# Kernel optimization log

Hardware: AMD Instinct MI355X
Metric: run time of the kernel (lower is better)

## Reference

```python
import math
import jax, jax.numpy as jnp
import numpy as np

NUM_HEADS = 16

def _alibi_slopes(n):
    def pow2(n):
        start = 2 ** (-2 ** (-(math.log2(n) - 3)))
        return [start * start ** i for i in range(n)]
    if math.log2(n).is_integer():
        return pow2(n)
    c = 2 ** math.floor(math.log2(n))
    return pow2(c) + _alibi_slopes(2 * c)[0::2][: n - c]

def _alibi_bias(num_heads, L):
    pos = np.arange(L)
    rel = (pos[None, :] - pos[:, None]).astype(np.float32)  # [L, L]
    slopes = np.asarray(_alibi_slopes(num_heads), dtype=np.float32)[:, None, None]
    bias = slopes * rel[None, :, :]  # [H, L, L]
    causal = pos[None, :] <= pos[:, None]
    bias = np.where(causal[None, :, :], bias, -np.inf).astype(np.float32)
    return jnp.asarray(bias)[None]  # [1, H, L, L]

def setup_inputs() -> dict:
    key = jax.random.key(0)
    ks = jax.random.split(key, 4)
    B, L, D = 2, 2048, 1024
    x = jax.random.normal(ks[0], (B, L, D), dtype=jnp.float32)
    W_in = jax.random.normal(ks[1], (D, 3 * D), dtype=jnp.float32) * 0.02
    b_in = jnp.zeros((3 * D,), dtype=jnp.float32)
    W_out = jax.random.normal(ks[2], (D, D), dtype=jnp.float32) * 0.02
    b_out = jnp.zeros((D,), dtype=jnp.float32)
    return {"x": x, "W_in": W_in, "b_in": b_in, "W_out": W_out, "b_out": b_out}

def reference(x, W_in, b_in, W_out, b_out):
    B, L, D = x.shape
    H = NUM_HEADS
    Dh = D // H
    qkv = x @ W_in + b_in  # [B, L, 3D]
    q, k, v = jnp.split(qkv, 3, axis=-1)
    # [B, H, L, Dh]
    q = q.reshape(B, L, H, Dh).transpose(0, 2, 1, 3)
    k = k.reshape(B, L, H, Dh).transpose(0, 2, 1, 3)
    v = v.reshape(B, L, H, Dh).transpose(0, 2, 1, 3)
    attn = jnp.einsum("bhqd,bhkd->bhqk", q, k) * (1.0 / math.sqrt(Dh))
    attn = attn + _alibi_bias(H, L)  # ALiBi + causal mask (-inf above diag)
    p = jax.nn.softmax(attn, axis=-1)
    out = jnp.einsum("bhqk,bhkd->bhqd", p, v)
    out = out.transpose(0, 2, 1, 3).reshape(B, L, D)
    out = out @ W_out + b_out
    return out, k, v
```

## Files before the change

kernel.cpp:

```cpp
#include <hip/hip_runtime.h>
#include <math.h>

typedef __bf16 bf16x8 __attribute__((ext_vector_type(8)));
typedef float  f32x4  __attribute__((ext_vector_type(4)));
typedef unsigned short u16x4 __attribute__((ext_vector_type(4)));

#define BATCH  2
#define SEQ    2048
#define DMODEL 1024
#define NHEAD  16
#define DHEAD  64
#define MROWS  4096
#define N_QKV  3072
#define KDIM   1024
#define OUTSECT (MROWS*DMODEL)

#define LOG2E 1.44269504088896f
#define QSCALE (0.125f * LOG2E)

__device__ inline __bf16 f2bf(float f) {
    unsigned u = __builtin_bit_cast(unsigned, f);
    unsigned r = (u + 0x7fffu + ((u >> 16) & 1u)) >> 16;
    return __builtin_bit_cast(__bf16, (unsigned short)r);
}

__device__ inline void gload16(const void* g, void* l) {
    __builtin_amdgcn_global_load_lds(
        (const __attribute__((address_space(1))) void*)g,
        (__attribute__((address_space(3))) void*)l, 16, 0, 0);
}

__device__ inline float dpp_max16(float x) {
    int v, t;
    v = __builtin_bit_cast(int, x);
    t = __builtin_amdgcn_update_dpp(v, v, 0xB1, 0xF, 0xF, false);
    x = fmaxf(x, __builtin_bit_cast(float, t));
    v = __builtin_bit_cast(int, x);
    t = __builtin_amdgcn_update_dpp(v, v, 0x4E, 0xF, 0xF, false);
    x = fmaxf(x, __builtin_bit_cast(float, t));
    v = __builtin_bit_cast(int, x);
    t = __builtin_amdgcn_update_dpp(v, v, 0x128, 0xF, 0xF, false);
    x = fmaxf(x, __builtin_bit_cast(float, t));
    v = __builtin_bit_cast(int, x);
    t = __builtin_amdgcn_update_dpp(v, v, 0x140, 0xF, 0xF, false);
    x = fmaxf(x, __builtin_bit_cast(float, t));
    return x;
}
__device__ inline float dpp_sum16(float x) {
    int v, t;
    v = __builtin_bit_cast(int, x);
    t = __builtin_amdgcn_update_dpp(v, v, 0xB1, 0xF, 0xF, false);
    x += __builtin_bit_cast(float, t);
    v = __builtin_bit_cast(int, x);
    t = __builtin_amdgcn_update_dpp(v, v, 0x4E, 0xF, 0xF, false);
    x += __builtin_bit_cast(float, t);
    v = __builtin_bit_cast(int, x);
    t = __builtin_amdgcn_update_dpp(v, v, 0x128, 0xF, 0xF, false);
    x += __builtin_bit_cast(float, t);
    v = __builtin_bit_cast(int, x);
    t = __builtin_amdgcn_update_dpp(v, v, 0x140, 0xF, 0xF, false);
    x += __builtin_bit_cast(float, t);
    return x;
}

__global__ __launch_bounds__(256) void cvt_all_k(
    const float* __restrict__ x, __bf16* __restrict__ xb,
    const float* __restrict__ W_in, __bf16* __restrict__ wti,
    const float* __restrict__ W_out, __bf16* __restrict__ wto)
{
    __shared__ float t[64][65];
    const int b = blockIdx.x;
    const int tid = threadIdx.x;
    if (b < 2048) {
        size_t i = (size_t)b * 256 + tid;
        const float4* p = (const float4*)x + i * 2;
        float4 a = p[0], c = p[1];
        __bf16 o[8] = {f2bf(a.x), f2bf(a.y), f2bf(a.z), f2bf(a.w),
                       f2bf(c.x), f2bf(c.y), f2bf(c.z), f2bf(c.w)};
        *(bf16x8*)(xb + i * 8) = *(bf16x8*)o;
        return;
    }
    const float* W;  __bf16* Wt;  int Nw, bx, by;
    if (b < 2816) { int c = b - 2048; W = W_in;  Wt = wti; Nw = N_QKV;  bx = c % 48; by = c / 48; }
    else          { int c = b - 2816; W = W_out; Wt = wto; Nw = DMODEL; bx = c % 16; by = c / 16; }
    const int k0 = by * 64, n0 = bx * 64;
    #pragma unroll
    for (int u = 0; u < 4; ++u) {
        int idx = u * 256 + tid;
        int r = idx >> 4, c4 = (idx & 15) << 2;
        float4 v = *(const float4*)&W[(size_t)(k0 + r) * Nw + n0 + c4];
        t[r][c4] = v.x; t[r][c4 + 1] = v.y; t[r][c4 + 2] = v.z; t[r][c4 + 3] = v.w;
    }
    __syncthreads();
    #pragma unroll
    for (int u = 0; u < 2; ++u) {
        int idx = u * 256 + tid;
        int n = idx >> 3, k8 = (idx & 7) << 3;
        __bf16 o[8];
        #pragma unroll
        for (int i = 0; i < 8; ++i) o[i] = f2bf(t[k8 + i][n]);
        *(bf16x8*)&Wt[(size_t)(n0 + n) * KDIM + k0 + k8] = *(bf16x8*)o;
    }
}

template<int MODE, int FI, int FJ>
__global__ __launch_bounds__(256) void gemm_bf(
    const __bf16* __restrict__ A, const __bf16* __restrict__ Bt,
    const float* __restrict__ bias,
    float* __restrict__ fo, float* __restrict__ kf, float* __restrict__ vf,
    __bf16* __restrict__ qb, __bf16* __restrict__ kb, __bf16* __restrict__ vb,
    int nbx)
{
    constexpr int BMt = FI * 32, BNt = FJ * 32;
    __shared__ __align__(16) __bf16 As[BMt * 64];
    __shared__ __align__(16) __bf16 Bs[BNt * 64];

    const int tid = threadIdx.x, wid = tid >> 6, lane = tid & 63;
    const int l16 = lane & 15, lq = lane >> 4;
    const int wm = wid >> 1, wn = wid & 1;

    const int nwg = gridDim.x;
    const int bid = blockIdx.x;
    const int swz = (bid & 7) * (nwg >> 3) + (bid >> 3);
    const int m0 = (swz / nbx) * BMt;
    const int n0 = (swz % nbx) * BNt;

    const int lr8 = lane >> 3;
    const int colE = ((lane & 7) ^ lr8) << 3;

    f32x4 acc[FI][FJ];
    #pragma unroll
    for (int i = 0; i < FI; ++i)
        #pragma unroll
        for (int j = 0; j < FJ; ++j)
            acc[i][j] = f32x4{0.f, 0.f, 0.f, 0.f};

    for (int k0 = 0; k0 < KDIM; k0 += 64) {
        __syncthreads();
        #pragma unroll
        for (int c = wid; c < FI * 4 + FJ * 4; c += 4) {
            const bool isA = (c < FI * 4);
            const int ch = isA ? c : c - FI * 4;
            const int row = ch * 8 + lr8;
            const __bf16* src = isA ? (A  + (size_t)(m0 + row) * KDIM + k0 + colE)
                                    : (Bt + (size_t)(n0 + row) * KDIM + k0 + colE);
            gload16(src, (isA ? As : Bs) + ch * 512);
        }
        __syncthreads();
        #pragma unroll
        for (int kk = 0; kk < 2; ++kk) {
            bf16x8 af[FI], bfg[FJ];
            #pragma unroll
            for (int i = 0; i < FI; ++i) {
                int r = wm * (FI * 16) + i * 16 + l16;
                af[i] = *(const bf16x8*)&As[r * 64 + ((kk * 32 + lq * 8) ^ ((r & 7) << 3))];
            }
            #pragma unroll
            for (int j = 0; j < FJ; ++j) {
                int r = wn * (FJ * 16) + j * 16 + l16;
                bfg[j] = *(const bf16x8*)&Bs[r * 64 + ((kk * 32 + lq * 8) ^ ((r & 7) << 3))];
            }
            #pragma unroll
            for (int i = 0; i < FI; ++i)
                #pragma unroll
                for (int j = 0; j < FJ; ++j)
                    acc[i][j] = __builtin_amdgcn_mfma_f32_16x16x32_bf16(af[i], bfg[j], acc[i][j], 0, 0, 0);
        }
    }

    #pragma unroll
    for (int i = 0; i < FI; ++i) {
        #pragma unroll
        for (int j = 0; j < FJ; ++j) {
            const int col  = n0 + wn * (FJ * 16) + j * 16 + l16;
            const int rowb = m0 + wm * (FI * 16) + i * 16 + lq * 4;
            float v[4];
            #pragma unroll
            for (int r = 0; r < 4; ++r) v[r] = acc[i][j][r] + bias[col];
            if (MODE == 1) {
                #pragma unroll
                for (int r = 0; r < 4; ++r)
                    fo[(size_t)(rowb + r) * DMODEL + col] = v[r];
            } else {
                const int which = col >> 10, rem = col & 1023;
                const int h = rem >> 6, dh = rem & 63;
                const int bb = rowb >> 11, ll = rowb & 2047;
                const size_t lidx = ((size_t)(bb * NHEAD + h) * SEQ + ll) * DHEAD + dh;
                if (which == 0) {
                    #pragma unroll
                    for (int r = 0; r < 4; ++r)
                        qb[lidx + (size_t)r * DHEAD] = f2bf(v[r] * QSCALE);
                } else if (which == 1) {
                    #pragma unroll
                    for (int r = 0; r < 4; ++r) {
                        kf[lidx + (size_t)r * DHEAD] = v[r];
                        kb[lidx + (size_t)r * DHEAD] = f2bf(v[r]);
                    }
                } else {
                    u16x4 pk;
                    #pragma unroll
                    for (int r = 0; r < 4; ++r) {
                        vf[lidx + (size_t)r * DHEAD] = v[r];
                        pk[r] = __builtin_bit_cast(unsigned short, f2bf(v[r]));
                    }
                    *(u16x4*)&vb[((size_t)(bb * NHEAD + h) * DHEAD + dh) * SEQ + ll] = pk;
                }
            }
        }
    }
}

__global__ __launch_bounds__(256) void attn_k(
    const __bf16* __restrict__ Qb, const __bf16* __restrict__ Kb,
    const __bf16* __restrict__ Vb, __bf16* __restrict__ Ob)
{
    __shared__ __align__(16) __bf16 Qs[64 * 64];
    __shared__ __align__(16) __bf16 Ks[2][64 * 64];
    __shared__ __align__(16) __bf16 Vs[2][64 * 64];
    __shared__ __align__(16) __bf16 Ps[4 * 16 * 64];

    const int tid = threadIdx.x, wid = tid >> 6, lane = tid & 63;
    const int l16 = lane & 15, lq = lane >> 4;

    const int bid = blockIdx.x;
    const int t   = bid >> 3;
    const int qt  = 31 - (t >> 2);
    const int bh  = (bid & 7) * 4 + (t & 3);
    const int h = bh & 15, bb = bh >> 4;
    const int q0 = qt * 64;
    const size_t kvbase = (size_t)bh * SEQ * DHEAD;
    const float slope2 = exp2f(-0.5f * (float)(h + 1)) * LOG2E;
    const int qr0 = wid * 16;
    const int lr8 = lane >> 3;
    const int colE = ((lane & 7) ^ lr8) << 3;

    #pragma unroll
    for (int u = 0; u < 2; ++u) {
        int ch = u * 4 + wid;
        int row = ch * 8 + lr8;
        gload16(Qb + kvbase + (size_t)(q0 + row) * DHEAD + colE, Qs + ch * 512);
    }
    #pragma unroll
    for (int u = 0; u < 2; ++u) {
        int ch = u * 4 + wid;
        int row = ch * 8 + lr8;
        gload16(Kb + kvbase + (size_t)row * DHEAD + colE, Ks[0] + ch * 512);
        gload16(Vb + kvbase + (size_t)row * SEQ  + colE, Vs[0] + ch * 512);
    }
    __syncthreads();

    float ct[4][4];
    #pragma unroll
    for (int r = 0; r < 4; ++r) {
        const int qi = q0 + qr0 + lq * 4 + r;
        #pragma unroll
        for (int nf = 0; nf < 4; ++nf)
            ct[r][nf] = slope2 * (float)(nf * 16 + l16 - qi);
    }
    const float dtj = slope2 * 64.f;

    float mrow[4], lrow[4];
    f32x4 accO[4];
    #pragma unroll
    for (int r = 0; r < 4; ++r) { mrow[r] = -1e30f; lrow[r] = 0.f; }
    #pragma unroll
    for (int j = 0; j < 4; ++j) accO[j] = f32x4{0.f, 0.f, 0.f, 0.f};

    int cur = 0;
    for (int jt = 0; jt <= qt; ++jt) {
        if (jt < qt) {
            const int jn = (jt + 1) * 64;
            #pragma unroll
            for (int u = 0; u < 2; ++u) {
                int ch = u * 4 + wid;
                int row = ch * 8 + lr8;
                gload16(Kb + kvbase + (size_t)(jn + row) * DHEAD + colE, Ks[cur ^ 1] + ch * 512);
                gload16(Vb + kvbase + (size_t)row * SEQ + jn + colE,     Vs[cur ^ 1] + ch * 512);
            }
        }

        const float tb = dtj * (float)jt;
        f32x4 s[4];
        #pragma unroll
        for (int nf = 0; nf < 4; ++nf) {
            #pragma unroll
            for (int r = 0; r < 4; ++r) s[nf][r] = ct[r][nf] + tb;
        }
        if (jt == qt) {
            #pragma unroll
            for (int nf = 0; nf < 4; ++nf)
                #pragma unroll
                for (int r = 0; r < 4; ++r)
                    if (nf * 16 + l16 > qr0 + lq * 4 + r) s[nf][r] = -3e38f;
        }

        const int qrow = qr0 + l16;
        bf16x8 aq0 = *(const bf16x8*)&Qs[qrow * 64 + ((lq * 8) ^ ((qrow & 7) << 3))];
        bf16x8 aq1 = *(const bf16x8*)&Qs[qrow * 64 + ((32 + lq * 8) ^ ((qrow & 7) << 3))];
        __builtin_amdgcn_s_setprio(1);
        #pragma unroll
        for (int nf = 0; nf < 4; ++nf) {
            int kr = nf * 16 + l16;
            bf16x8 bk0 = *(const bf16x8*)&Ks[cur][kr * 64 + ((lq * 8) ^ ((kr & 7) << 3))];
            bf16x8 bk1 = *(const bf16x8*)&Ks[cur][kr * 64 + ((32 + lq * 8) ^ ((kr & 7) << 3))];
            s[nf] = __builtin_amdgcn_mfma_f32_16x16x32_bf16(aq0, bk0, s[nf], 0, 0, 0);
            s[nf] = __builtin_amdgcn_mfma_f32_16x16x32_bf16(aq1, bk1, s[nf], 0, 0, 0);
        }
        __builtin_amdgcn_s_setprio(0);

        float rm[4];
        #pragma unroll
        for (int r = 0; r < 4; ++r)
            rm[r] = dpp_max16(fmaxf(fmaxf(s[0][r], s[1][r]), fmaxf(s[2][r], s[3][r])));
        bool need = (rm[0] > mrow[0] + 8.f) || (rm[1] > mrow[1] + 8.f) ||
                    (rm[2] > mrow[2] + 8.f) || (rm[3] > mrow[3] + 8.f);
        if (__any(need)) {
            #pragma unroll
            for (int r = 0; r < 4; ++r) {
                float mnew = fmaxf(mrow[r], rm[r]);
                float scale = __builtin_amdgcn_exp2f(mrow[r] - mnew);
                lrow[r] *= scale;
                mrow[r] = mnew;
                #pragma unroll
                for (int nf = 0; nf < 4; ++nf) accO[nf][r] *= scale;
            }
        }
        #pragma unroll
        for (int r = 0; r < 4; ++r) {
            float p0 = __builtin_amdgcn_exp2f(s[0][r] - mrow[r]);
            float p1 = __builtin_amdgcn_exp2f(s[1][r] - mrow[r]);
            float p2 = __builtin_amdgcn_exp2f(s[2][r] - mrow[r]);
            float p3 = __builtin_amdgcn_exp2f(s[3][r] - mrow[r]);
            const int prow = lq * 4 + r;
            const int pb = wid * 1024 + prow * 64;
            const int px = (prow & 7) << 3;
            Ps[pb + ((l16     ) ^ px)] = (__bf16)p0;
            Ps[pb + ((l16 + 16) ^ px)] = (__bf16)p1;
            Ps[pb + ((l16 + 32) ^ px)] = (__bf16)p2;
            Ps[pb + ((l16 + 48) ^ px)] = (__bf16)p3;
            lrow[r] += dpp_sum16((p0 + p1) + (p2 + p3));
        }

        bf16x8 ap0 = *(const bf16x8*)&Ps[wid * 1024 + l16 * 64 + ((lq * 8) ^ ((l16 & 7) << 3))];
        bf16x8 ap1 = *(const bf16x8*)&Ps[wid * 1024 + l16 * 64 + ((32 + lq * 8) ^ ((l16 & 7) << 3))];
        __builtin_amdgcn_s_setprio(1);
        #pragma unroll
        for (int nf = 0; nf < 4; ++nf) {
            int vr = nf * 16 + l16;
            bf16x8 bv0 = *(const bf16x8*)&Vs[cur][vr * 64 + ((lq * 8) ^ ((vr & 7) << 3))];
            bf16x8 bv1 = *(const bf16x8*)&Vs[cur][vr * 64 + ((32 + lq * 8) ^ ((vr & 7) << 3))];
            accO[nf] = __builtin_amdgcn_mfma_f32_16x16x32_bf16(ap0, bv0, accO[nf], 0, 0, 0);
            accO[nf] = __builtin_amdgcn_mfma_f32_16x16x32_bf16(ap1, bv1, accO[nf], 0, 0, 0);
        }
        __builtin_amdgcn_s_setprio(0);

        __syncthreads();
        cur ^= 1;
    }

    #pragma unroll
    for (int r = 0; r < 4; ++r) {
        const float inv = __builtin_amdgcn_rcpf(lrow[r]);
        const int qi = q0 + qr0 + lq * 4 + r;
        #pragma unroll
        for (int nf = 0; nf < 4; ++nf) {
            int dh = nf * 16 + l16;
            Ob[(size_t)(bb * SEQ + qi) * DMODEL + h * DHEAD + dh] = (__bf16)(accO[nf][r] * inv);
        }
    }
}

extern "C" void kernel_launch(void* const* d_in, const int* in_sizes, int n_in,
                              void* d_out, int out_size, void* d_ws, size_t ws_size,
                              hipStream_t stream) {
    const float* x     = (const float*)d_in[0];
    const float* W_in  = (const float*)d_in[1];
    const float* b_in  = (const float*)d_in[2];
    const float* W_out = (const float*)d_in[3];
    const float* b_out = (const float*)d_in[4];

    float* out = (float*)d_out;
    float* kf  = out + (size_t)OUTSECT;
    float* vf  = out + 2 * (size_t)OUTSECT;

    __bf16* qb = (__bf16*)d_out;
    __bf16* xb = (__bf16*)d_out + (size_t)OUTSECT;

    __bf16* ob  = (__bf16*)d_ws;
    __bf16* kb  = ob + (size_t)OUTSECT;
    __bf16* vb  = kb + (size_t)OUTSECT;
    __bf16* wti = vb + (size_t)OUTSECT;
    __bf16* wto = wti + (size_t)N_QKV * KDIM;

    cvt_all_k<<<3072, 256, 0, stream>>>(x, xb, W_in, wti, W_out, wto);

    gemm_bf<0, 4, 4><<<768, 256, 0, stream>>>(xb, wti, b_in,
        nullptr, kf, vf, qb, kb, vb, N_QKV / 128);

    attn_k<<<1024, 256, 0, stream>>>(qb, kb, vb, ob);

    gemm_bf<1, 4, 4><<<256, 256, 0, stream>>>(ob, wto, b_out,
        out, nullptr, nullptr, nullptr, nullptr, nullptr, DMODEL / 128);
}
```

Baseline: 199.9 us.

## Use 128-row query tiles with 8 waves sharing each K/V tile

The attention kernel now processes 128 query rows per block with 512 threads (8 waves), so each loaded K/V tile is reused by twice as many query rows. This halves global K/V traffic per query. The block schedule pairs a long and a short query tile (half flag) to balance causal work. Q fragments are hoisted out of the loop, and waves whose rows lie entirely above the current key tile skip compute but still join the barrier, which leaves some idle waves on the diagonal tiles.

```diff
diff --git a/kernel.cpp b/kernel.cpp
--- a/kernel.cpp
+++ b/kernel.cpp
@@ -210,49 +210,54 @@
     }
 }
 
-__global__ __launch_bounds__(256) void attn_k(
+__global__ __launch_bounds__(512) void attn_k(
     const __bf16* __restrict__ Qb, const __bf16* __restrict__ Kb,
     const __bf16* __restrict__ Vb, __bf16* __restrict__ Ob)
 {
-    __shared__ __align__(16) __bf16 Qs[64 * 64];
+    __shared__ __align__(16) __bf16 Qs[128 * 64];
     __shared__ __align__(16) __bf16 Ks[2][64 * 64];
     __shared__ __align__(16) __bf16 Vs[2][64 * 64];
-    __shared__ __align__(16) __bf16 Ps[4 * 16 * 64];
+    __shared__ __align__(16) __bf16 Ps[8 * 16 * 64];
 
     const int tid = threadIdx.x, wid = tid >> 6, lane = tid & 63;
     const int l16 = lane & 15, lq = lane >> 4;
 
     const int bid = blockIdx.x;
-    const int t   = bid >> 3;
-    const int qt  = 31 - (t >> 2);
-    const int bh  = (bid & 7) * 4 + (t & 3);
+    const int j   = bid >> 3;
+    const int p   = j >> 1, half = j & 1;
+    const int bh  = (bid & 7) * 4 + (p & 3);
+    const int q2i = p >> 2;
+    const int qt2 = half ? q2i : (15 - q2i);
     const int h = bh & 15, bb = bh >> 4;
-    const int q0 = qt * 64;
+    const int q0b  = qt2 * 128;
+    const int jtop = 2 * qt2 + 1;
     const size_t kvbase = (size_t)bh * SEQ * DHEAD;
     const float slope2 = exp2f(-0.5f * (float)(h + 1)) * LOG2E;
-    const int qr0 = wid * 16;
+    const int qa = q0b + wid * 16;
     const int lr8 = lane >> 3;
     const int colE = ((lane & 7) ^ lr8) << 3;
 
     #pragma unroll
     for (int u = 0; u < 2; ++u) {
-        int ch = u * 4 + wid;
+        int ch = wid * 2 + u;
         int row = ch * 8 + lr8;
-        gload16(Qb + kvbase + (size_t)(q0 + row) * DHEAD + colE, Qs + ch * 512);
-    }
-    #pragma unroll
-    for (int u = 0; u < 2; ++u) {
-        int ch = u * 4 + wid;
-        int row = ch * 8 + lr8;
-        gload16(Kb + kvbase + (size_t)row * DHEAD + colE, Ks[0] + ch * 512);
-        gload16(Vb + kvbase + (size_t)row * SEQ  + colE, Vs[0] + ch * 512);
+        gload16(Qb + kvbase + (size_t)(q0b + row) * DHEAD + colE, Qs + ch * 512);
+    }
+    {
+        int row = wid * 8 + lr8;
+        gload16(Kb + kvbase + (size_t)row * DHEAD + colE, Ks[0] + wid * 512);
+        gload16(Vb + kvbase + (size_t)row * SEQ  + colE, Vs[0] + wid * 512);
     }
     __syncthreads();
 
+    const int qrow = wid * 16 + l16;
+    const bf16x8 aq0 = *(const bf16x8*)&Qs[qrow * 64 + ((lq * 8) ^ ((qrow & 7) << 3))];
+    const bf16x8 aq1 = *(const bf16x8*)&Qs[qrow * 64 + ((32 + lq * 8) ^ ((qrow & 7) << 3))];
+
     float ct[4][4];
     #pragma unroll
     for (int r = 0; r < 4; ++r) {
-        const int qi = q0 + qr0 + lq * 4 + r;
+        const int qi = qa + lq * 4 + r;
         #pragma unroll
         for (int nf = 0; nf < 4; ++nf)
             ct[r][nf] = slope2 * (float)(nf * 16 + l16 - qi);
@@ -264,95 +269,92 @@
     #pragma unroll
     for (int r = 0; r < 4; ++r) { mrow[r] = -1e30f; lrow[r] = 0.f; }
     #pragma unroll
-    for (int j = 0; j < 4; ++j) accO[j] = f32x4{0.f, 0.f, 0.f, 0.f};
+    for (int jj = 0; jj < 4; ++jj) accO[jj] = f32x4{0.f, 0.f, 0.f, 0.f};
 
     int cur = 0;
-    for (int jt = 0; jt <= qt; ++jt) {
-        if (jt < qt) {
-            const int jn = (jt + 1) * 64;
-            #pragma unroll
-            for (int u = 0; u < 2; ++u) {
-                int ch = u * 4 + wid;
-                int row = ch * 8 + lr8;
-                gload16(Kb + kvbase + (size_t)(jn + row) * DHEAD + colE, Ks[cur ^ 1] + ch * 512);
-                gload16(Vb + kvbase + (size_t)row * SEQ + jn + colE,     Vs[cur ^ 1] + ch * 512);
-            }
-        }
-
-        const float tb = dtj * (float)jt;
-        f32x4 s[4];
-        #pragma unroll
-        for (int nf = 0; nf < 4; ++nf) {
-            #pragma unroll
-            for (int r = 0; r < 4; ++r) s[nf][r] = ct[r][nf] + tb;
-        }
-        if (jt == qt) {
+    for (int jt = 0; jt <= jtop; ++jt) {
+        const int j0 = jt * 64;
+
+        if (jt < jtop) {
+            const int jn = j0 + 64;
+            int row = wid * 8 + lr8;
+            gload16(Kb + kvbase + (size_t)(jn + row) * DHEAD + colE, Ks[cur ^ 1] + wid * 512);
+            gload16(Vb + kvbase + (size_t)row * SEQ + jn + colE,     Vs[cur ^ 1] + wid * 512);
+        }
+
+        if (qa + 16 > j0) {
+            const float tb = dtj * (float)jt;
+            f32x4 s[4];
             #pragma unroll
             for (int nf = 0; nf < 4; ++nf)
                 #pragma unroll
-                for (int r = 0; r < 4; ++r)
-                    if (nf * 16 + l16 > qr0 + lq * 4 + r) s[nf][r] = -3e38f;
-        }
-
-        const int qrow = qr0 + l16;
-        bf16x8 aq0 = *(const bf16x8*)&Qs[qrow * 64 + ((lq * 8) ^ ((qrow & 7) << 3))];
-        bf16x8 aq1 = *(const bf16x8*)&Qs[qrow * 64 + ((32 + lq * 8) ^ ((qrow & 7) << 3))];
-        __builtin_amdgcn_s_setprio(1);
-        #pragma unroll
-        for (int nf = 0; nf < 4; ++nf) {
-            int kr = nf * 16 + l16;
-            bf16x8 bk0 = *(const bf16x8*)&Ks[cur][kr * 64 + ((lq * 8) ^ ((kr & 7) << 3))];
-            bf16x8 bk1 = *(const bf16x8*)&Ks[cur][kr * 64 + ((32 + lq * 8) ^ ((kr & 7) << 3))];
-            s[nf] = __builtin_amdgcn_mfma_f32_16x16x32_bf16(aq0, bk0, s[nf], 0, 0, 0);
-            s[nf] = __builtin_amdgcn_mfma_f32_16x16x32_bf16(aq1, bk1, s[nf], 0, 0, 0);
-        }
-        __builtin_amdgcn_s_setprio(0);
-
-        float rm[4];
-        #pragma unroll
-        for (int r = 0; r < 4; ++r)
-            rm[r] = dpp_max16(fmaxf(fmaxf(s[0][r], s[1][r]), fmaxf(s[2][r], s[3][r])));
-        bool need = (rm[0] > mrow[0] + 8.f) || (rm[1] > mrow[1] + 8.f) ||
-                    (rm[2] > mrow[2] + 8.f) || (rm[3] > mrow[3] + 8.f);
-        if (__any(need)) {
+                for (int r = 0; r < 4; ++r) s[nf][r] = ct[r][nf] + tb;
+            if (qa < j0 + 64) {
+                const int rel = qa - j0;
+                #pragma unroll
+                for (int nf = 0; nf < 4; ++nf)
+                    #pragma unroll
+                    for (int r = 0; r < 4; ++r)
+                        if (nf * 16 + l16 > rel + lq * 4 + r) s[nf][r] = -3e38f;
+            }
+
+            __builtin_amdgcn_s_setprio(1);
+            #pragma unroll
+            for (int nf = 0; nf < 4; ++nf) {
+                int kr = nf * 16 + l16;
+                bf16x8 bk0 = *(const bf16x8*)&Ks[cur][kr * 64 + ((lq * 8) ^ ((kr & 7) << 3))];
+                bf16x8 bk1 = *(const bf16x8*)&Ks[cur][kr * 64 + ((32 + lq * 8) ^ ((kr & 7) << 3))];
+                s[nf] = __builtin_amdgcn_mfma_f32_16x16x32_bf16(aq0, bk0, s[nf], 0, 0, 0);
+                s[nf] = __builtin_amdgcn_mfma_f32_16x16x32_bf16(aq1, bk1, s[nf], 0, 0, 0);
+            }
+            __builtin_amdgcn_s_setprio(0);
+
+            float rm[4];
+            #pragma unroll
+            for (int r = 0; r < 4; ++r)
+                rm[r] = dpp_max16(fmaxf(fmaxf(s[0][r], s[1][r]), fmaxf(s[2][r], s[3][r])));
+            bool need = (rm[0] > mrow[0] + 8.f) || (rm[1] > mrow[1] + 8.f) ||
+                        (rm[2] > mrow[2] + 8.f) || (rm[3] > mrow[3] + 8.f);
+            if (__any(need)) {
+                #pragma unroll
+                for (int r = 0; r < 4; ++r) {
+                    float mnew = fmaxf(mrow[r], rm[r]);
+                    float scale = __builtin_amdgcn_exp2f(mrow[r] - mnew);
+                    lrow[r] *= scale;
+                    mrow[r] = mnew;
+                    #pragma unroll
+                    for (int nf = 0; nf < 4; ++nf) accO[nf][r] *= scale;
+                }
+            }
             #pragma unroll
             for (int r = 0; r < 4; ++r) {
-                float mnew = fmaxf(mrow[r], rm[r]);
-                float scale = __builtin_amdgcn_exp2f(mrow[r] - mnew);
-                lrow[r] *= scale;
-                mrow[r] = mnew;
-                #pragma unroll
-                for (int nf = 0; nf < 4; ++nf) accO[nf][r] *= scale;
-            }
-        }
-        #pragma unroll
-        for (int r = 0; r < 4; ++r) {
-            float p0 = __builtin_amdgcn_exp2f(s[0][r] - mrow[r]);
-            float p1 = __builtin_amdgcn_exp2f(s[1][r] - mrow[r]);
-            float p2 = __builtin_amdgcn_exp2f(s[2][r] - mrow[r]);
-            float p3 = __builtin_amdgcn_exp2f(s[3][r] - mrow[r]);
-            const int prow = lq * 4 + r;
-            const int pb = wid * 1024 + prow * 64;
-            const int px = (prow & 7) << 3;
-            Ps[pb + ((l16     ) ^ px)] = (__bf16)p0;
-            Ps[pb + ((l16 + 16) ^ px)] = (__bf16)p1;
-            Ps[pb + ((l16 + 32) ^ px)] = (__bf16)p2;
-            Ps[pb + ((l16 + 48) ^ px)] = (__bf16)p3;
-            lrow[r] += dpp_sum16((p0 + p1) + (p2 + p3));
-        }
-
-        bf16x8 ap0 = *(const bf16x8*)&Ps[wid * 1024 + l16 * 64 + ((lq * 8) ^ ((l16 & 7) << 3))];
-        bf16x8 ap1 = *(const bf16x8*)&Ps[wid * 1024 + l16 * 64 + ((32 + lq * 8) ^ ((l16 & 7) << 3))];
-        __builtin_amdgcn_s_setprio(1);
-        #pragma unroll
-        for (int nf = 0; nf < 4; ++nf) {
-            int vr = nf * 16 + l16;
-            bf16x8 bv0 = *(const bf16x8*)&Vs[cur][vr * 64 + ((lq * 8) ^ ((vr & 7) << 3))];
-            bf16x8 bv1 = *(const bf16x8*)&Vs[cur][vr * 64 + ((32 + lq * 8) ^ ((vr & 7) << 3))];
-            accO[nf] = __builtin_amdgcn_mfma_f32_16x16x32_bf16(ap0, bv0, accO[nf], 0, 0, 0);
-            accO[nf] = __builtin_amdgcn_mfma_f32_16x16x32_bf16(ap1, bv1, accO[nf], 0, 0, 0);
-        }
-        __builtin_amdgcn_s_setprio(0);
+                float p0 = __builtin_amdgcn_exp2f(s[0][r] - mrow[r]);
+                float p1 = __builtin_amdgcn_exp2f(s[1][r] - mrow[r]);
+                float p2 = __builtin_amdgcn_exp2f(s[2][r] - mrow[r]);
+                float p3 = __builtin_amdgcn_exp2f(s[3][r] - mrow[r]);
+                const int prow = lq * 4 + r;
+                const int pb = wid * 1024 + prow * 64;
+                const int px = (prow & 7) << 3;
+                Ps[pb + ((l16     ) ^ px)] = (__bf16)p0;
+                Ps[pb + ((l16 + 16) ^ px)] = (__bf16)p1;
+                Ps[pb + ((l16 + 32) ^ px)] = (__bf16)p2;
+                Ps[pb + ((l16 + 48) ^ px)] = (__bf16)p3;
+                lrow[r] += dpp_sum16((p0 + p1) + (p2 + p3));
+            }
+
+            bf16x8 ap0 = *(const bf16x8*)&Ps[wid * 1024 + l16 * 64 + ((lq * 8) ^ ((l16 & 7) << 3))];
+            bf16x8 ap1 = *(const bf16x8*)&Ps[wid * 1024 + l16 * 64 + ((32 + lq * 8) ^ ((l16 & 7) << 3))];
+            __builtin_amdgcn_s_setprio(1);
+            #pragma unroll
+            for (int nf = 0; nf < 4; ++nf) {
+                int vr = nf * 16 + l16;
+                bf16x8 bv0 = *(const bf16x8*)&Vs[cur][vr * 64 + ((lq * 8) ^ ((vr & 7) << 3))];
+                bf16x8 bv1 = *(const bf16x8*)&Vs[cur][vr * 64 + ((32 + lq * 8) ^ ((vr & 7) << 3))];
+                accO[nf] = __builtin_amdgcn_mfma_f32_16x16x32_bf16(ap0, bv0, accO[nf], 0, 0, 0);
+                accO[nf] = __builtin_amdgcn_mfma_f32_16x16x32_bf16(ap1, bv1, accO[nf], 0, 0, 0);
+            }
+            __builtin_amdgcn_s_setprio(0);
+        }
 
         __syncthreads();
         cur ^= 1;
@@ -361,7 +363,7 @@
     #pragma unroll
     for (int r = 0; r < 4; ++r) {
         const float inv = __builtin_amdgcn_rcpf(lrow[r]);
-        const int qi = q0 + qr0 + lq * 4 + r;
+        const int qi = qa + lq * 4 + r;
         #pragma unroll
         for (int nf = 0; nf < 4; ++nf) {
             int dh = nf * 16 + l16;
@@ -397,7 +399,7 @@
     gemm_bf<0, 4, 4><<<768, 256, 0, stream>>>(xb, wti, b_in,
         nullptr, kf, vf, qb, kb, vb, N_QKV / 128);
 
-    attn_k<<<1024, 256, 0, stream>>>(qb, kb, vb, ob);
+    attn_k<<<512, 512, 0, stream>>>(qb, kb, vb, ob);
 
     gemm_bf<1, 4, 4><<<256, 256, 0, stream>>>(ob, wto, b_out,
         out, nullptr, nullptr, nullptr, nullptr, nullptr, DMODEL / 128);
```

Result: slower. 215.8 us (+8.0%).
